# Kernel optimization log

Hardware: AMD Instinct MI355X
Metric: run time of the kernel (lower is better)

The kernel has to match this reference:

```python
import jax, jax.numpy as jnp
import numpy as np

B, S, D, H = 65536, 5, 128, 8  # batch, seq_len(=5, fixed by property_bias), d_model, heads
HD = D // H                     # head_dim = 16


def setup_inputs() -> dict:
    key = jax.random.key(0)
    ks = jax.random.split(key, 9)
    scale = 0.02
    x = jax.random.normal(ks[0], (B, S, D), jnp.float32)
    Wq = jax.random.normal(ks[1], (D, D), jnp.float32) * scale
    Wk = jax.random.normal(ks[2], (D, D), jnp.float32) * scale
    Wv = jax.random.normal(ks[3], (D, D), jnp.float32) * scale
    Wo = jax.random.normal(ks[4], (D, D), jnp.float32) * scale
    bq = jnp.zeros((D,), jnp.float32)
    bk = jnp.zeros((D,), jnp.float32)
    bv = jnp.zeros((D,), jnp.float32)
    bo = jnp.zeros((D,), jnp.float32)
    # property bias init: zeros except head 0 attends to last property (melting point)
    pbias = jnp.zeros((H, S, S), jnp.float32).at[0, :, -1].set(1.0)
    return {"x": x, "Wq": Wq, "bq": bq, "Wk": Wk, "bk": bk,
            "Wv": Wv, "bv": bv, "Wo": Wo, "bo": bo, "pbias": pbias}


def reference(x, Wq, bq, Wk, bk, Wv, bv, Wo, bo, pbias):
    b, s, d = x.shape
    h = pbias.shape[0]
    hd = d // h
    # projections, split into heads: [b, h, s, hd]
    q = (x @ Wq + bq).reshape(b, s, h, hd).transpose(0, 2, 1, 3)
    k = (x @ Wk + bk).reshape(b, s, h, hd).transpose(0, 2, 1, 3)
    v = (x @ Wv + bv).reshape(b, s, h, hd).transpose(0, 2, 1, 3)
    # scaled dot-product scores + additive per-head property bias
    scores = jnp.einsum('bhsd,bhtd->bhst', q, k) / jnp.sqrt(jnp.float32(hd))
    scores = scores + pbias[None]  # broadcast over batch
    attn = jax.nn.softmax(scores, axis=-1)  # dropout p=0.0 (eval) -> identity
    out = jnp.einsum('bhst,bhtd->bhsd', attn, v)
    out = out.transpose(0, 2, 1, 3).reshape(b, s, d)
    return out @ Wo + bo
```

## Files before the change

kernel.cpp:

```cpp
#include <hip/hip_runtime.h>

typedef _Float16 f16;
typedef _Float16 f16x2 __attribute__((ext_vector_type(2)));
typedef _Float16 f16x4 __attribute__((ext_vector_type(4)));
typedef _Float16 f16x8 __attribute__((ext_vector_type(8)));
typedef float f32x4 __attribute__((ext_vector_type(4)));

#define NB 65536

__device__ __align__(16) f16 g_WT[4][128][128];

__global__ void k_wtrans(const float* __restrict__ Wq, const float* __restrict__ Wk,
                         const float* __restrict__ Wv, const float* __restrict__ Wo) {
    int tid = blockIdx.x * 256 + threadIdx.x;
    int m = tid >> 14;
    int r = tid & 16383;
    int n = r >> 7;
    int k = r & 127;
    const float* W = (m == 0) ? Wq : (m == 1) ? Wk : (m == 2) ? Wv : Wo;
    g_WT[m][n][k] = (f16)W[k * 128 + n];
}

__device__ __forceinline__ f16x2 bc2(unsigned u) {
    union { unsigned u; f16x2 h; } x; x.u = u; return x.h;
}
__device__ __forceinline__ f16x8 cat8(f16x4 lo, f16x4 hi) {
    f16x8 r;
    r[0] = lo[0]; r[1] = lo[1]; r[2] = lo[2]; r[3] = lo[3];
    r[4] = hi[0]; r[5] = hi[1]; r[6] = hi[2]; r[7] = hi[3];
    return r;
}

__global__ __launch_bounds__(512, 4)
void k_fused(const float* __restrict__ x, const float* __restrict__ bq,
             const float* __restrict__ bk, const float* __restrict__ bv,
             const float* __restrict__ bo, const float* __restrict__ pbias,
             float* __restrict__ out) {
    __shared__ __align__(16) f16 QKVs[3][8][80][16];
    __shared__ float pb_l[200];

    const int tid  = threadIdx.x;
    const int w    = tid >> 6;
    const int lane = tid & 63;
    const int c    = lane & 15;
    const int g    = lane >> 4;
    const int base = blockIdx.x * 80;
    const int key_c = (c >> 2) & 3;

    if (tid < 200) pb_l[tid] = pbias[tid];

    f16x8 wA[3][4];
#pragma unroll
    for (int ks = 0; ks < 4; ++ks) {
        wA[0][ks] = *(const f16x8*)&g_WT[0][w * 16 + c][ks * 32 + g * 8];
        wA[1][ks] = *(const f16x8*)&g_WT[1][w * 16 + c][ks * 32 + g * 8];
        wA[2][ks] = *(const f16x8*)&g_WT[2][w * 16 + c][ks * 32 + g * 8];
    }
    float4 bq4 = *(const float4*)&bq[w * 16 + g * 4];
    float4 bk4 = *(const float4*)&bk[w * 16 + g * 4];
    float4 bv4 = *(const float4*)&bv[w * 16 + g * 4];

#pragma unroll 1
    for (int t = 0; t < 5; ++t) {
        const float* xr = x + (size_t)(base + t * 16 + c) * 128;
        f32x4 qa = {0.f, 0.f, 0.f, 0.f}, ka = {0.f, 0.f, 0.f, 0.f}, va = {0.f, 0.f, 0.f, 0.f};
#pragma unroll
        for (int ks = 0; ks < 4; ++ks) {
            float4 u0 = *(const float4*)(xr + ks * 32 + g * 8);
            float4 u1 = *(const float4*)(xr + ks * 32 + g * 8 + 4);
            f16x8 bx;
            bx[0] = (f16)u0.x; bx[1] = (f16)u0.y; bx[2] = (f16)u0.z; bx[3] = (f16)u0.w;
            bx[4] = (f16)u1.x; bx[5] = (f16)u1.y; bx[6] = (f16)u1.z; bx[7] = (f16)u1.w;
            qa = __builtin_amdgcn_mfma_f32_16x16x32_f16(wA[0][ks], bx, qa, 0, 0, 0);
            ka = __builtin_amdgcn_mfma_f32_16x16x32_f16(wA[1][ks], bx, ka, 0, 0, 0);
            va = __builtin_amdgcn_mfma_f32_16x16x32_f16(wA[2][ks], bx, va, 0, 0, 0);
        }
        int row  = t * 16 + c;
        int slot = g ^ key_c;
        f16x4 qh, kh, vh;
        qh[0] = (f16)(qa[0] + bq4.x); qh[1] = (f16)(qa[1] + bq4.y);
        qh[2] = (f16)(qa[2] + bq4.z); qh[3] = (f16)(qa[3] + bq4.w);
        kh[0] = (f16)(ka[0] + bk4.x); kh[1] = (f16)(ka[1] + bk4.y);
        kh[2] = (f16)(ka[2] + bk4.z); kh[3] = (f16)(ka[3] + bk4.w);
        vh[0] = (f16)(va[0] + bv4.x); vh[1] = (f16)(va[1] + bv4.y);
        vh[2] = (f16)(va[2] + bv4.z); vh[3] = (f16)(va[3] + bv4.w);
        *(f16x4*)&QKVs[0][w][row][slot * 4] = qh;
        *(f16x4*)&QKVs[1][w][row][slot * 4] = kh;
        *(f16x4*)&QKVs[2][w][row][slot * 4] = vh;
    }
    __syncthreads();

#pragma unroll 1
    for (int pass = 0; pass < 2; ++pass) {
        int task = lane + pass * 64;
        if (task < 80) {
            int row = task;
            int b5  = row / 5;
            int qi  = row - b5 * 5;
            int kr0 = b5 * 5;
            int key = (row >> 2) & 3;

            uint2 qw0 = *(const uint2*)&QKVs[0][w][row][(0 ^ key) * 4];
            uint2 qw1 = *(const uint2*)&QKVs[0][w][row][(1 ^ key) * 4];
            uint2 qw2 = *(const uint2*)&QKVs[0][w][row][(2 ^ key) * 4];
            uint2 qw3 = *(const uint2*)&QKVs[0][w][row][(3 ^ key) * 4];
            f16x2 q0 = bc2(qw0.x), q1 = bc2(qw0.y), q2 = bc2(qw1.x), q3 = bc2(qw1.y);
            f16x2 q4 = bc2(qw2.x), q5 = bc2(qw2.y), q6 = bc2(qw3.x), q7 = bc2(qw3.y);

            float s[5];
#pragma unroll
            for (int j = 0; j < 5; ++j) {
                int kr = kr0 + j;
                int kk = (kr >> 2) & 3;
                uint2 k0 = *(const uint2*)&QKVs[1][w][kr][(0 ^ kk) * 4];
                uint2 k1 = *(const uint2*)&QKVs[1][w][kr][(1 ^ kk) * 4];
                uint2 k2 = *(const uint2*)&QKVs[1][w][kr][(2 ^ kk) * 4];
                uint2 k3 = *(const uint2*)&QKVs[1][w][kr][(3 ^ kk) * 4];
                float d = 0.f;
                d = __builtin_amdgcn_fdot2(q0, bc2(k0.x), d, false);
                d = __builtin_amdgcn_fdot2(q1, bc2(k0.y), d, false);
                d = __builtin_amdgcn_fdot2(q2, bc2(k1.x), d, false);
                d = __builtin_amdgcn_fdot2(q3, bc2(k1.y), d, false);
                d = __builtin_amdgcn_fdot2(q4, bc2(k2.x), d, false);
                d = __builtin_amdgcn_fdot2(q5, bc2(k2.y), d, false);
                d = __builtin_amdgcn_fdot2(q6, bc2(k3.x), d, false);
                d = __builtin_amdgcn_fdot2(q7, bc2(k3.y), d, false);
                s[j] = d * 0.25f + pb_l[w * 25 + qi * 5 + j];
            }
            float mx = fmaxf(fmaxf(fmaxf(s[0], s[1]), fmaxf(s[2], s[3])), s[4]);
            float psum = 0.f;
#pragma unroll
            for (int j = 0; j < 5; ++j) { s[j] = __expf(s[j] - mx); psum += s[j]; }
            float inv = 1.0f / psum;

            float o[16];
#pragma unroll
            for (int i = 0; i < 16; ++i) o[i] = 0.f;
#pragma unroll
            for (int j = 0; j < 5; ++j) {
                int kr = kr0 + j;
                int kk = (kr >> 2) & 3;
                uint2 v0 = *(const uint2*)&QKVs[2][w][kr][(0 ^ kk) * 4];
                uint2 v1 = *(const uint2*)&QKVs[2][w][kr][(1 ^ kk) * 4];
                uint2 v2 = *(const uint2*)&QKVs[2][w][kr][(2 ^ kk) * 4];
                uint2 v3 = *(const uint2*)&QKVs[2][w][kr][(3 ^ kk) * 4];
                float p = s[j] * inv;
                f16x2 a;
                a = bc2(v0.x); o[0]  += p * (float)a[0]; o[1]  += p * (float)a[1];
                a = bc2(v0.y); o[2]  += p * (float)a[0]; o[3]  += p * (float)a[1];
                a = bc2(v1.x); o[4]  += p * (float)a[0]; o[5]  += p * (float)a[1];
                a = bc2(v1.y); o[6]  += p * (float)a[0]; o[7]  += p * (float)a[1];
                a = bc2(v2.x); o[8]  += p * (float)a[0]; o[9]  += p * (float)a[1];
                a = bc2(v2.y); o[10] += p * (float)a[0]; o[11] += p * (float)a[1];
                a = bc2(v3.x); o[12] += p * (float)a[0]; o[13] += p * (float)a[1];
                a = bc2(v3.y); o[14] += p * (float)a[0]; o[15] += p * (float)a[1];
            }
            f16x4 oc;
            oc[0] = (f16)o[0];  oc[1] = (f16)o[1];  oc[2] = (f16)o[2];  oc[3] = (f16)o[3];
            *(f16x4*)&QKVs[0][w][row][(0 ^ key) * 4] = oc;
            oc[0] = (f16)o[4];  oc[1] = (f16)o[5];  oc[2] = (f16)o[6];  oc[3] = (f16)o[7];
            *(f16x4*)&QKVs[0][w][row][(1 ^ key) * 4] = oc;
            oc[0] = (f16)o[8];  oc[1] = (f16)o[9];  oc[2] = (f16)o[10]; oc[3] = (f16)o[11];
            *(f16x4*)&QKVs[0][w][row][(2 ^ key) * 4] = oc;
            oc[0] = (f16)o[12]; oc[1] = (f16)o[13]; oc[2] = (f16)o[14]; oc[3] = (f16)o[15];
            *(f16x4*)&QKVs[0][w][row][(3 ^ key) * 4] = oc;
        }
    }
    __syncthreads();

    f16x8 wo[4];
#pragma unroll
    for (int ks = 0; ks < 4; ++ks)
        wo[ks] = *(const f16x8*)&g_WT[3][w * 16 + c][ks * 32 + g * 8];
    float4 bo4 = *(const float4*)&bo[w * 16 + g * 4];
    const int hh_b = g >> 1;
    const int c0   = (g & 1) * 2;
#pragma unroll 1
    for (int t = 0; t < 5; ++t) {
        int row = t * 16 + c;
        f32x4 acc = {0.f, 0.f, 0.f, 0.f};
#pragma unroll
        for (int ks = 0; ks < 4; ++ks) {
            int hh = ks * 2 + hh_b;
            f16x4 lo = *(const f16x4*)&QKVs[0][hh][row][((c0 ^ key_c)) * 4];
            f16x4 hi = *(const f16x4*)&QKVs[0][hh][row][(((c0 + 1) ^ key_c)) * 4];
            acc = __builtin_amdgcn_mfma_f32_16x16x32_f16(wo[ks], cat8(lo, hi), acc, 0, 0, 0);
        }
        float4 r;
        r.x = acc[0] + bo4.x; r.y = acc[1] + bo4.y;
        r.z = acc[2] + bo4.z; r.w = acc[3] + bo4.w;
        *(float4*)&out[(size_t)(base + row) * 128 + w * 16 + g * 4] = r;
    }
}

extern "C" void kernel_launch(void* const* d_in, const int* in_sizes, int n_in,
                              void* d_out, int out_size, void* d_ws, size_t ws_size,
                              hipStream_t stream) {
    const float* x     = (const float*)d_in[0];
    const float* Wq    = (const float*)d_in[1];
    const float* bq    = (const float*)d_in[2];
    const float* Wk    = (const float*)d_in[3];
    const float* bk    = (const float*)d_in[4];
    const float* Wv    = (const float*)d_in[5];
    const float* bv    = (const float*)d_in[6];
    const float* Wo    = (const float*)d_in[7];
    const float* bo    = (const float*)d_in[8];
    const float* pbias = (const float*)d_in[9];
    float* out = (float*)d_out;

    k_wtrans<<<dim3(256), dim3(256), 0, stream>>>(Wq, Wk, Wv, Wo);
    k_fused<<<dim3(NB / 16), dim3(512), 0, stream>>>(x, bq, bk, bv, bo, pbias, out);
}
```

Measured before the change: 438.4 us.

## Drop intra-wave barrier, preload pbias to registers, pack f16 conversions, nontemporal stores

Removes the barrier between the QKV projection and attention, since each wave reads only its own head's slice of shared memory. Pbias now goes into registers instead of shared memory. F32 to f16 conversions use packed cvt_pkrtz, and the P·V accumulation is done in packed f16 rather than f32. The projection and output loops are fully unrolled, and output writes use nontemporal stores. Together these aim to cut synchronization, ALU and conversion work, at the cost of lower precision in the attention output and higher register pressure.

```diff
diff --git a/kernel.cpp b/kernel.cpp
--- a/kernel.cpp
+++ b/kernel.cpp
@@ -4,7 +4,9 @@
 typedef _Float16 f16x2 __attribute__((ext_vector_type(2)));
 typedef _Float16 f16x4 __attribute__((ext_vector_type(4)));
 typedef _Float16 f16x8 __attribute__((ext_vector_type(8)));
+typedef __fp16 h16x2 __attribute__((ext_vector_type(2)));
 typedef float f32x4 __attribute__((ext_vector_type(4)));
+typedef float fltx4 __attribute__((ext_vector_type(4)));
 
 #define NB 65536
 
@@ -24,6 +26,11 @@
 __device__ __forceinline__ f16x2 bc2(unsigned u) {
     union { unsigned u; f16x2 h; } x; x.u = u; return x.h;
 }
+__device__ __forceinline__ f16x2 pkh(float a, float b) {
+    union { h16x2 a; f16x2 b; } u;
+    u.a = __builtin_amdgcn_cvt_pkrtz(a, b);
+    return u.b;
+}
 __device__ __forceinline__ f16x8 cat8(f16x4 lo, f16x4 hi) {
     f16x8 r;
     r[0] = lo[0]; r[1] = lo[1]; r[2] = lo[2]; r[3] = lo[3];
@@ -37,7 +44,6 @@
              const float* __restrict__ bo, const float* __restrict__ pbias,
              float* __restrict__ out) {
     __shared__ __align__(16) f16 QKVs[3][8][80][16];
-    __shared__ float pb_l[200];
 
     const int tid  = threadIdx.x;
     const int w    = tid >> 6;
@@ -47,8 +53,6 @@
     const int base = blockIdx.x * 80;
     const int key_c = (c >> 2) & 3;
 
-    if (tid < 200) pb_l[tid] = pbias[tid];
-
     f16x8 wA[3][4];
 #pragma unroll
     for (int ks = 0; ks < 4; ++ks) {
@@ -60,7 +64,18 @@
     float4 bk4 = *(const float4*)&bk[w * 16 + g * 4];
     float4 bv4 = *(const float4*)&bv[w * 16 + g * 4];
 
-#pragma unroll 1
+    const int rowA = lane;
+    const int b5A  = rowA / 5, qiA = rowA - b5A * 5;
+    const int rowB = 64 + lane;
+    const int b5B  = rowB / 5, qiB = rowB - b5B * 5;
+    float pbA[5], pbB[5];
+#pragma unroll
+    for (int j = 0; j < 5; ++j) {
+        pbA[j] = pbias[w * 25 + qiA * 5 + j];
+        pbB[j] = pbias[w * 25 + qiB * 5 + j];
+    }
+
+#pragma unroll
     for (int t = 0; t < 5; ++t) {
         const float* xr = x + (size_t)(base + t * 16 + c) * 128;
         f32x4 qa = {0.f, 0.f, 0.f, 0.f}, ka = {0.f, 0.f, 0.f, 0.f}, va = {0.f, 0.f, 0.f, 0.f};
@@ -68,114 +83,102 @@
         for (int ks = 0; ks < 4; ++ks) {
             float4 u0 = *(const float4*)(xr + ks * 32 + g * 8);
             float4 u1 = *(const float4*)(xr + ks * 32 + g * 8 + 4);
-            f16x8 bx;
-            bx[0] = (f16)u0.x; bx[1] = (f16)u0.y; bx[2] = (f16)u0.z; bx[3] = (f16)u0.w;
-            bx[4] = (f16)u1.x; bx[5] = (f16)u1.y; bx[6] = (f16)u1.z; bx[7] = (f16)u1.w;
-            qa = __builtin_amdgcn_mfma_f32_16x16x32_f16(wA[0][ks], bx, qa, 0, 0, 0);
-            ka = __builtin_amdgcn_mfma_f32_16x16x32_f16(wA[1][ks], bx, ka, 0, 0, 0);
-            va = __builtin_amdgcn_mfma_f32_16x16x32_f16(wA[2][ks], bx, va, 0, 0, 0);
+            union { f16x8 v; f16x2 h[4]; } bx;
+            bx.h[0] = pkh(u0.x, u0.y); bx.h[1] = pkh(u0.z, u0.w);
+            bx.h[2] = pkh(u1.x, u1.y); bx.h[3] = pkh(u1.z, u1.w);
+            qa = __builtin_amdgcn_mfma_f32_16x16x32_f16(wA[0][ks], bx.v, qa, 0, 0, 0);
+            ka = __builtin_amdgcn_mfma_f32_16x16x32_f16(wA[1][ks], bx.v, ka, 0, 0, 0);
+            va = __builtin_amdgcn_mfma_f32_16x16x32_f16(wA[2][ks], bx.v, va, 0, 0, 0);
         }
         int row  = t * 16 + c;
         int slot = g ^ key_c;
-        f16x4 qh, kh, vh;
-        qh[0] = (f16)(qa[0] + bq4.x); qh[1] = (f16)(qa[1] + bq4.y);
-        qh[2] = (f16)(qa[2] + bq4.z); qh[3] = (f16)(qa[3] + bq4.w);
-        kh[0] = (f16)(ka[0] + bk4.x); kh[1] = (f16)(ka[1] + bk4.y);
-        kh[2] = (f16)(ka[2] + bk4.z); kh[3] = (f16)(ka[3] + bk4.w);
-        vh[0] = (f16)(va[0] + bv4.x); vh[1] = (f16)(va[1] + bv4.y);
-        vh[2] = (f16)(va[2] + bv4.z); vh[3] = (f16)(va[3] + bv4.w);
-        *(f16x4*)&QKVs[0][w][row][slot * 4] = qh;
-        *(f16x4*)&QKVs[1][w][row][slot * 4] = kh;
-        *(f16x4*)&QKVs[2][w][row][slot * 4] = vh;
-    }
-    __syncthreads();
-
-#pragma unroll 1
-    for (int pass = 0; pass < 2; ++pass) {
-        int task = lane + pass * 64;
-        if (task < 80) {
-            int row = task;
-            int b5  = row / 5;
-            int qi  = row - b5 * 5;
-            int kr0 = b5 * 5;
-            int key = (row >> 2) & 3;
-
-            uint2 qw0 = *(const uint2*)&QKVs[0][w][row][(0 ^ key) * 4];
-            uint2 qw1 = *(const uint2*)&QKVs[0][w][row][(1 ^ key) * 4];
-            uint2 qw2 = *(const uint2*)&QKVs[0][w][row][(2 ^ key) * 4];
-            uint2 qw3 = *(const uint2*)&QKVs[0][w][row][(3 ^ key) * 4];
-            f16x2 q0 = bc2(qw0.x), q1 = bc2(qw0.y), q2 = bc2(qw1.x), q3 = bc2(qw1.y);
-            f16x2 q4 = bc2(qw2.x), q5 = bc2(qw2.y), q6 = bc2(qw3.x), q7 = bc2(qw3.y);
-
-            float s[5];
-#pragma unroll
-            for (int j = 0; j < 5; ++j) {
-                int kr = kr0 + j;
-                int kk = (kr >> 2) & 3;
-                uint2 k0 = *(const uint2*)&QKVs[1][w][kr][(0 ^ kk) * 4];
-                uint2 k1 = *(const uint2*)&QKVs[1][w][kr][(1 ^ kk) * 4];
-                uint2 k2 = *(const uint2*)&QKVs[1][w][kr][(2 ^ kk) * 4];
-                uint2 k3 = *(const uint2*)&QKVs[1][w][kr][(3 ^ kk) * 4];
-                float d = 0.f;
-                d = __builtin_amdgcn_fdot2(q0, bc2(k0.x), d, false);
-                d = __builtin_amdgcn_fdot2(q1, bc2(k0.y), d, false);
-                d = __builtin_amdgcn_fdot2(q2, bc2(k1.x), d, false);
-                d = __builtin_amdgcn_fdot2(q3, bc2(k1.y), d, false);
-                d = __builtin_amdgcn_fdot2(q4, bc2(k2.x), d, false);
-                d = __builtin_amdgcn_fdot2(q5, bc2(k2.y), d, false);
-                d = __builtin_amdgcn_fdot2(q6, bc2(k3.x), d, false);
-                d = __builtin_amdgcn_fdot2(q7, bc2(k3.y), d, false);
-                s[j] = d * 0.25f + pb_l[w * 25 + qi * 5 + j];
-            }
-            float mx = fmaxf(fmaxf(fmaxf(s[0], s[1]), fmaxf(s[2], s[3])), s[4]);
-            float psum = 0.f;
-#pragma unroll
-            for (int j = 0; j < 5; ++j) { s[j] = __expf(s[j] - mx); psum += s[j]; }
-            float inv = 1.0f / psum;
-
-            float o[16];
-#pragma unroll
-            for (int i = 0; i < 16; ++i) o[i] = 0.f;
-#pragma unroll
-            for (int j = 0; j < 5; ++j) {
-                int kr = kr0 + j;
-                int kk = (kr >> 2) & 3;
-                uint2 v0 = *(const uint2*)&QKVs[2][w][kr][(0 ^ kk) * 4];
-                uint2 v1 = *(const uint2*)&QKVs[2][w][kr][(1 ^ kk) * 4];
-                uint2 v2 = *(const uint2*)&QKVs[2][w][kr][(2 ^ kk) * 4];
-                uint2 v3 = *(const uint2*)&QKVs[2][w][kr][(3 ^ kk) * 4];
-                float p = s[j] * inv;
-                f16x2 a;
-                a = bc2(v0.x); o[0]  += p * (float)a[0]; o[1]  += p * (float)a[1];
-                a = bc2(v0.y); o[2]  += p * (float)a[0]; o[3]  += p * (float)a[1];
-                a = bc2(v1.x); o[4]  += p * (float)a[0]; o[5]  += p * (float)a[1];
-                a = bc2(v1.y); o[6]  += p * (float)a[0]; o[7]  += p * (float)a[1];
-                a = bc2(v2.x); o[8]  += p * (float)a[0]; o[9]  += p * (float)a[1];
-                a = bc2(v2.y); o[10] += p * (float)a[0]; o[11] += p * (float)a[1];
-                a = bc2(v3.x); o[12] += p * (float)a[0]; o[13] += p * (float)a[1];
-                a = bc2(v3.y); o[14] += p * (float)a[0]; o[15] += p * (float)a[1];
-            }
-            f16x4 oc;
-            oc[0] = (f16)o[0];  oc[1] = (f16)o[1];  oc[2] = (f16)o[2];  oc[3] = (f16)o[3];
-            *(f16x4*)&QKVs[0][w][row][(0 ^ key) * 4] = oc;
-            oc[0] = (f16)o[4];  oc[1] = (f16)o[5];  oc[2] = (f16)o[6];  oc[3] = (f16)o[7];
-            *(f16x4*)&QKVs[0][w][row][(1 ^ key) * 4] = oc;
-            oc[0] = (f16)o[8];  oc[1] = (f16)o[9];  oc[2] = (f16)o[10]; oc[3] = (f16)o[11];
-            *(f16x4*)&QKVs[0][w][row][(2 ^ key) * 4] = oc;
-            oc[0] = (f16)o[12]; oc[1] = (f16)o[13]; oc[2] = (f16)o[14]; oc[3] = (f16)o[15];
-            *(f16x4*)&QKVs[0][w][row][(3 ^ key) * 4] = oc;
-        }
-    }
-    __syncthreads();
+        union { f16x4 v; f16x2 h[2]; } st;
+        st.h[0] = pkh(qa[0] + bq4.x, qa[1] + bq4.y);
+        st.h[1] = pkh(qa[2] + bq4.z, qa[3] + bq4.w);
+        *(f16x4*)&QKVs[0][w][row][slot * 4] = st.v;
+        st.h[0] = pkh(ka[0] + bk4.x, ka[1] + bk4.y);
+        st.h[1] = pkh(ka[2] + bk4.z, ka[3] + bk4.w);
+        *(f16x4*)&QKVs[1][w][row][slot * 4] = st.v;
+        st.h[0] = pkh(va[0] + bv4.x, va[1] + bv4.y);
+        st.h[1] = pkh(va[2] + bv4.z, va[3] + bv4.w);
+        *(f16x4*)&QKVs[2][w][row][slot * 4] = st.v;
+    }
+
+    auto attn = [&](int row, int b5, const float* pb) {
+        const int key = (row >> 2) & 3;
+        const int kr0 = b5 * 5;
+
+        uint2 qw0 = *(const uint2*)&QKVs[0][w][row][(0 ^ key) * 4];
+        uint2 qw1 = *(const uint2*)&QKVs[0][w][row][(1 ^ key) * 4];
+        uint2 qw2 = *(const uint2*)&QKVs[0][w][row][(2 ^ key) * 4];
+        uint2 qw3 = *(const uint2*)&QKVs[0][w][row][(3 ^ key) * 4];
+        f16x2 q0 = bc2(qw0.x), q1 = bc2(qw0.y), q2 = bc2(qw1.x), q3 = bc2(qw1.y);
+        f16x2 q4 = bc2(qw2.x), q5 = bc2(qw2.y), q6 = bc2(qw3.x), q7 = bc2(qw3.y);
+
+        float s[5];
+#pragma unroll
+        for (int j = 0; j < 5; ++j) {
+            int kr = kr0 + j;
+            int kk = (kr >> 2) & 3;
+            uint2 k0 = *(const uint2*)&QKVs[1][w][kr][(0 ^ kk) * 4];
+            uint2 k1 = *(const uint2*)&QKVs[1][w][kr][(1 ^ kk) * 4];
+            uint2 k2 = *(const uint2*)&QKVs[1][w][kr][(2 ^ kk) * 4];
+            uint2 k3 = *(const uint2*)&QKVs[1][w][kr][(3 ^ kk) * 4];
+            float d = 0.f;
+            d = __builtin_amdgcn_fdot2(q0, bc2(k0.x), d, false);
+            d = __builtin_amdgcn_fdot2(q1, bc2(k0.y), d, false);
+            d = __builtin_amdgcn_fdot2(q2, bc2(k1.x), d, false);
+            d = __builtin_amdgcn_fdot2(q3, bc2(k1.y), d, false);
+            d = __builtin_amdgcn_fdot2(q4, bc2(k2.x), d, false);
+            d = __builtin_amdgcn_fdot2(q5, bc2(k2.y), d, false);
+            d = __builtin_amdgcn_fdot2(q6, bc2(k3.x), d, false);
+            d = __builtin_amdgcn_fdot2(q7, bc2(k3.y), d, false);
+            s[j] = d * 0.25f + pb[j];
+        }
+        float mx = fmaxf(fmaxf(fmaxf(s[0], s[1]), fmaxf(s[2], s[3])), s[4]);
+        float psum = 0.f;
+#pragma unroll
+        for (int j = 0; j < 5; ++j) { s[j] = __expf(s[j] - mx); psum += s[j]; }
+        float inv = 1.0f / psum;
+
+        f16x2 o2[8];
+#pragma unroll
+        for (int i = 0; i < 8; ++i) { o2[i][0] = (f16)0.f; o2[i][1] = (f16)0.f; }
+#pragma unroll
+        for (int j = 0; j < 5; ++j) {
+            int kr = kr0 + j;
+            int kk = (kr >> 2) & 3;
+            uint2 v0 = *(const uint2*)&QKVs[2][w][kr][(0 ^ kk) * 4];
+            uint2 v1 = *(const uint2*)&QKVs[2][w][kr][(1 ^ kk) * 4];
+            uint2 v2 = *(const uint2*)&QKVs[2][w][kr][(2 ^ kk) * 4];
+            uint2 v3 = *(const uint2*)&QKVs[2][w][kr][(3 ^ kk) * 4];
+            f16 pf = (f16)(s[j] * inv);
+            f16x2 p2; p2[0] = pf; p2[1] = pf;
+            o2[0] += p2 * bc2(v0.x); o2[1] += p2 * bc2(v0.y);
+            o2[2] += p2 * bc2(v1.x); o2[3] += p2 * bc2(v1.y);
+            o2[4] += p2 * bc2(v2.x); o2[5] += p2 * bc2(v2.y);
+            o2[6] += p2 * bc2(v3.x); o2[7] += p2 * bc2(v3.y);
+        }
+        union { f16x4 v; f16x2 h[2]; } st;
+        st.h[0] = o2[0]; st.h[1] = o2[1]; *(f16x4*)&QKVs[0][w][row][(0 ^ key) * 4] = st.v;
+        st.h[0] = o2[2]; st.h[1] = o2[3]; *(f16x4*)&QKVs[0][w][row][(1 ^ key) * 4] = st.v;
+        st.h[0] = o2[4]; st.h[1] = o2[5]; *(f16x4*)&QKVs[0][w][row][(2 ^ key) * 4] = st.v;
+        st.h[0] = o2[6]; st.h[1] = o2[7]; *(f16x4*)&QKVs[0][w][row][(3 ^ key) * 4] = st.v;
+    };
+    attn(rowA, b5A, pbA);
+    if (lane < 16) attn(rowB, b5B, pbB);
 
     f16x8 wo[4];
 #pragma unroll
     for (int ks = 0; ks < 4; ++ks)
         wo[ks] = *(const f16x8*)&g_WT[3][w * 16 + c][ks * 32 + g * 8];
     float4 bo4 = *(const float4*)&bo[w * 16 + g * 4];
+
+    __syncthreads();
+
     const int hh_b = g >> 1;
     const int c0   = (g & 1) * 2;
-#pragma unroll 1
+#pragma unroll
     for (int t = 0; t < 5; ++t) {
         int row = t * 16 + c;
         f32x4 acc = {0.f, 0.f, 0.f, 0.f};
@@ -186,10 +189,10 @@
             f16x4 hi = *(const f16x4*)&QKVs[0][hh][row][(((c0 + 1) ^ key_c)) * 4];
             acc = __builtin_amdgcn_mfma_f32_16x16x32_f16(wo[ks], cat8(lo, hi), acc, 0, 0, 0);
         }
-        float4 r;
-        r.x = acc[0] + bo4.x; r.y = acc[1] + bo4.y;
-        r.z = acc[2] + bo4.z; r.w = acc[3] + bo4.w;
-        *(float4*)&out[(size_t)(base + row) * 128 + w * 16 + g * 4] = r;
+        fltx4 r;
+        r[0] = acc[0] + bo4.x; r[1] = acc[1] + bo4.y;
+        r[2] = acc[2] + bo4.z; r[3] = acc[3] + bo4.w;
+        __builtin_nontemporal_store(r, (fltx4*)&out[(size_t)(base + row) * 128 + w * 16 + g * 4]);
     }
 }
 
```

Result: slower. 491.5 us (+12.1%).
